# Optimization experiments

Hardware: AMD Instinct MI355X
Metric: run time of the kernel (lower is better)

Reference implementation:

```python
import jax, jax.numpy as jnp
import numpy as np

NEG_SLOPE = 0.2


def _gat_layer(x, edge_index, W, a_src, a_dst, b):
    """PyG GATConv: linear -> per-edge attention logits -> segment softmax over
    destination -> scatter-add weighted messages. Self-loops added (PyG default)."""
    N = x.shape[0]
    heads, out = a_src.shape
    loops = jnp.arange(N, dtype=edge_index.dtype)
    src = jnp.concatenate([edge_index[0], loops])
    dst = jnp.concatenate([edge_index[1], loops])
    xh = (x @ W).reshape(N, heads, out)                      # [N,H,D]
    alpha_s = (xh * a_src).sum(-1)                           # [N,H]
    alpha_d = (xh * a_dst).sum(-1)                           # [N,H]
    e = jax.nn.leaky_relu(alpha_s[src] + alpha_d[dst], NEG_SLOPE)  # [E,H]
    emax = jax.ops.segment_max(e, dst, num_segments=N)       # [N,H]
    ex = jnp.exp(e - emax[dst])
    den = jax.ops.segment_sum(ex, dst, num_segments=N)
    att = ex / (den[dst] + 1e-16)                            # [E,H]
    msg = xh[src] * att[..., None]                           # [E,H,D]
    o = jax.ops.segment_sum(msg, dst, num_segments=N)        # [N,H,D]
    return o.reshape(N, heads * out) + b


def _single_source_gnn(h, edge_index, params):
    n_layers = len(params)
    for i, (W, a_s, a_d, b) in enumerate(params):
        h = _gat_layer(h, edge_index, W, a_s, a_d, b)
        if i < n_layers - 1:
            h = jax.nn.relu(h)
    return h


def setup_inputs() -> dict:
    key = jax.random.key(0)
    B, N, H, heads, deg = 4, 2000, 64, 4, 32
    E = N * deg
    ks = jax.random.split(key, 20)

    def mk_edge_index(k):
        e = jax.random.randint(k, (2, B, E), 0, N)
        off = (jnp.arange(B) * N)[None, :, None]
        return (e + off).reshape(2, B * E).astype(jnp.int32)

    inp = {
        "h0_flat": jax.random.normal(ks[0], (B * N, H), jnp.float32),
        "edge_index_s1": mk_edge_index(ks[1]),
        "edge_index_s2": mk_edge_index(ks[2]),
    }
    dims = [(H, H * heads), (H * heads, H * heads)]
    i = 3
    for s in ("s1", "s2"):
        for l, (din, dout) in enumerate(dims):
            inp[f"W_{s}_{l}"] = jax.random.normal(ks[i], (din, dout), jnp.float32) * 0.1; i += 1
            inp[f"a_src_{s}_{l}"] = jax.random.normal(ks[i], (heads, H), jnp.float32) * 0.1; i += 1
            inp[f"a_dst_{s}_{l}"] = jax.random.normal(ks[i], (heads, H), jnp.float32) * 0.1; i += 1
            inp[f"b_{s}_{l}"] = jnp.zeros((dout,), jnp.float32)
    inp["batch_size"] = B
    inp["num_stocks"] = N
    return inp


def reference(h0_flat, edge_index_s1, edge_index_s2,
              W_s1_0, a_src_s1_0, a_dst_s1_0, b_s1_0,
              W_s1_1, a_src_s1_1, a_dst_s1_1, b_s1_1,
              W_s2_0, a_src_s2_0, a_dst_s2_0, b_s2_0,
              W_s2_1, a_src_s2_1, a_dst_s2_1, b_s2_1,
              batch_size, num_stocks):
    p1 = [(W_s1_0, a_src_s1_0, a_dst_s1_0, b_s1_0),
          (W_s1_1, a_src_s1_1, a_dst_s1_1, b_s1_1)]
    p2 = [(W_s2_0, a_src_s2_0, a_dst_s2_0, b_s2_0),
          (W_s2_1, a_src_s2_1, a_dst_s2_1, b_s2_1)]
    h1 = _single_source_gnn(h0_flat, edge_index_s1, p1)
    h2 = _single_source_gnn(h0_flat, edge_index_s2, p2)
    # dict of per-source outputs in torch -> stacked [n_sources, B*N, H*heads]
    return jnp.stack([h1, h2])
```

## Files before the change

kernel.cpp:

```cpp
#include <hip/hip_runtime.h>
#include <hip/hip_fp16.h>


#define NEG_SLOPE 0.2f
#define ELLW 96

typedef _Float16 half8 __attribute__((ext_vector_type(8)));
typedef float floatx4 __attribute__((ext_vector_type(4)));


__global__ __launch_bounds__(64) void wt_zero_kernel(
        const float* __restrict__ W10, const float* __restrict__ W20,
        const float* __restrict__ W11, const float* __restrict__ W21,
        _Float16* __restrict__ Wt10, _Float16* __restrict__ Wt20,
        _Float16* __restrict__ Wt11, _Float16* __restrict__ Wt21,
        int* __restrict__ cnt, int twoN) {
    int z = blockIdx.z, y = blockIdx.y, c = blockIdx.x;
    int t = threadIdx.x;
    int flat = ((z * gridDim.y + y) * gridDim.x + c) * 64 + t;
    if (flat < twoN) cnt[flat] = 0;
    if (y == 0) {
        const float* W  = z ? W20  : W10;
        _Float16*    Wt = z ? Wt20 : Wt10;
        Wt[(size_t)c * 64 + t] = (_Float16)W[(size_t)t * 256 + c];
    } else {
        int k = (y - 1) * 64 + t;
        const float* W  = z ? W21  : W11;
        _Float16*    Wt = z ? Wt21 : Wt11;
        Wt[(size_t)c * 256 + k] = (_Float16)W[(size_t)k * 256 + c];
    }
}


__global__ __launch_bounds__(256) void scatter_ell_kernel(
        const int* __restrict__ ei1, int E1,
        const int* __restrict__ ei2, int E2, int N,
        int* __restrict__ cnt , int* __restrict__ slots ) {
    int i = blockIdx.x * 256 + threadIdx.x;
    int tot1 = E1 + N;
    int tot2 = E2 + N;
    if (i >= tot1 + tot2) return;
    int s, j; const int* ei; int E;
    if (i < tot1) { s = 0; j = i;        ei = ei1; E = E1; }
    else          { s = 1; j = i - tot1; ei = ei2; E = E2; }
    int src, dst;
    if (j < E) { src = ei[j]; dst = ei[E + j]; }
    else       { src = dst = j - E; }
    int g = s * N + dst;
    int pos = atomicAdd(&cnt[g], 1);
    if (pos < ELLW) slots[(size_t)g * ELLW + pos] = src;
}


#define BK 64
#define HPAD 4

struct GemmArgs {
    const float *h0, *h1;
    const _Float16 *Wt0, *Wt1;
    const float *as0, *as1, *ad0, *ad1;
    __half *xh0, *xh1;
    float *alS0, *alS1, *alD0, *alD1;
    int K;
};

__global__ __launch_bounds__(256) void gemm_mfma_kernel(GemmArgs g) {
    __shared__ _Float16 hT[32][BK + HPAD];
    int s = blockIdx.z;
    const float*    h   = s ? g.h1   : g.h0;
    const _Float16* Wt  = s ? g.Wt1  : g.Wt0;
    const float*    a_s = s ? g.as1  : g.as0;
    const float*    a_d = s ? g.ad1  : g.ad0;
    __half* xh = s ? g.xh1 : g.xh0;
    float* alS = s ? g.alS1 : g.alS0;
    float* alD = s ? g.alD1 : g.alD0;
    const int K = g.K;

    int tid  = threadIdx.x;
    int wave = tid >> 6;
    int lane = tid & 63;
    int lo = lane & 15, hi = lane >> 4;
    int row0 = blockIdx.x * 32;
    int c0 = wave * 64;

    floatx4 acc[2][4] = {};

    int srow = tid >> 3, sseg = tid & 7;
    const float* hrow = h + (size_t)(row0 + srow) * K + sseg * 8;
    const _Float16* wbase = Wt + (size_t)c0 * K;

    for (int k0 = 0; k0 < K; k0 += BK) {
        __syncthreads();
        float4 hv0 = *(const float4*)(hrow + k0);
        float4 hv1 = *(const float4*)(hrow + k0 + 4);
        half8 hh;
        hh[0] = (_Float16)hv0.x; hh[1] = (_Float16)hv0.y;
        hh[2] = (_Float16)hv0.z; hh[3] = (_Float16)hv0.w;
        hh[4] = (_Float16)hv1.x; hh[5] = (_Float16)hv1.y;
        hh[6] = (_Float16)hv1.z; hh[7] = (_Float16)hv1.w;
        *(half8*)&hT[srow][sseg * 8] = hh;
        __syncthreads();

        half8 bf[2][4], af[2][2];
#pragma unroll
        for (int ks = 0; ks < 2; ks++) {
#pragma unroll
            for (int cf = 0; cf < 4; cf++) {
                bf[ks][cf] = *(const half8*)(wbase + (size_t)(cf * 16 + lo) * K
                                             + k0 + ks * 32 + hi * 8);
            }
#pragma unroll
            for (int f = 0; f < 2; f++)
                af[ks][f] = *(const half8*)&hT[f * 16 + lo][ks * 32 + hi * 8];
        }
#pragma unroll
        for (int ks = 0; ks < 2; ks++)
#pragma unroll
            for (int f = 0; f < 2; f++)
#pragma unroll
                for (int cf = 0; cf < 4; cf++)
                    acc[f][cf] = __builtin_amdgcn_mfma_f32_16x16x32_f16(
                        af[ks][f], bf[ks][cf], acc[f][cf], 0, 0, 0);
    }

    float asw[4], adw[4];
#pragma unroll
    for (int cf = 0; cf < 4; cf++) {
        asw[cf] = a_s[c0 + cf * 16 + lo];
        adw[cf] = a_d[c0 + cf * 16 + lo];
    }
#pragma unroll
    for (int f = 0; f < 2; f++) {
#pragma unroll
        for (int r = 0; r < 4; r++) {
            int row = row0 + f * 16 + hi * 4 + r;
            float v0 = acc[f][0][r], v1 = acc[f][1][r];
            float v2 = acc[f][2][r], v3 = acc[f][3][r];
            __half* xrow = &xh[(size_t)row * 256 + c0 + lo];
            xrow[0]  = __float2half(v0);
            xrow[16] = __float2half(v1);
            xrow[32] = __float2half(v2);
            xrow[48] = __float2half(v3);
            float s1 = v0 * asw[0] + v1 * asw[1] + v2 * asw[2] + v3 * asw[3];
            float s2 = v0 * adw[0] + v1 * adw[1] + v2 * adw[2] + v3 * adw[3];
#pragma unroll
            for (int off = 1; off < 16; off <<= 1) {
                s1 += __shfl_xor(s1, off);
                s2 += __shfl_xor(s2, off);
            }
            if (lo == 0) {
                alS[row * 4 + wave] = s1;
                alD[row * 4 + wave] = s2;
            }
        }
    }
}


struct AttnArgs {
    const int *cnt, *slots;
    const __half *xh0, *xh1;
    const float *alS0, *alS1, *alD0, *alD1, *b0, *b1;
    float *out0, *out1;
    int N, do_relu;
};

__global__ __launch_bounds__(256) void attn_kernel(AttnArgs a) {
    __shared__ float2 pairs[4][8][10];
    int tid = threadIdx.x;
    int h  = tid >> 6;
    int L  = tid & 63;
    int st = L >> 3;
    int lc = L & 7;
    int g = blockIdx.x;
    int s = (g >= a.N) ? 1 : 0;
    int dst = g - s * a.N;
    const __half* xh     = s ? a.xh1  : a.xh0;
    const float*  alS    = s ? a.alS1 : a.alS0;
    const float*  alD    = s ? a.alD1 : a.alD0;
    const float*  bias   = s ? a.b1   : a.b0;
    float*        out    = s ? a.out1 : a.out0;

    int nd = a.cnt[g];
    if (nd > ELLW) nd = ELLW;
    const int* slots = a.slots + (size_t)g * ELLW;
    float ad = alD[dst * 4 + h];
    const char* xb = (const char*)xh + h * 128 + lc * 16;

    float acc[8] = {};
    float pden = 0.f;

    for (int c = 0; c < nd; c += 64) {
        int n = nd - c; if (n > 64) n = 64;
        int off = 0; float p = 0.f;
        if (L < n) {
            int src = slots[c + L];
            float t = alS[src * 4 + h] + ad;
            t = (t > 0.f) ? t : NEG_SLOPE * t;
            p = __expf(t);
            off = src * 512;
        }
        pden += p;
        pairs[h][L & 7][L >> 3] = make_float2(__int_as_float(off), p);
        int iters = (n + 7) >> 3;
        for (int ii = 0; ii < iters; ii += 4) {
            float4 twoA = *(const float4*)&pairs[h][st][ii];
            float4 twoB = *(const float4*)&pairs[h][st][ii + 2];
            int   o0 = __float_as_int(twoA.x); float w0 = twoA.y;
            int   o1 = __float_as_int(twoA.z); float w1 = twoA.w;
            int   o2 = __float_as_int(twoB.x); float w2 = twoB.y;
            int   o3 = __float_as_int(twoB.z); float w3 = twoB.w;
            float4 r0 = *(const float4*)(xb + o0);
            float4 r1 = *(const float4*)(xb + o1);
            float4 r2 = *(const float4*)(xb + o2);
            float4 r3 = *(const float4*)(xb + o3);
            const __half2* q0 = (const __half2*)&r0;
            const __half2* q1 = (const __half2*)&r1;
            const __half2* q2 = (const __half2*)&r2;
            const __half2* q3 = (const __half2*)&r3;
#pragma unroll
            for (int k = 0; k < 4; k++) {
                acc[2 * k + 0] += (float)q0[k].x * w0;
                acc[2 * k + 1] += (float)q0[k].y * w0;
            }
#pragma unroll
            for (int k = 0; k < 4; k++) {
                acc[2 * k + 0] += (float)q1[k].x * w1;
                acc[2 * k + 1] += (float)q1[k].y * w1;
            }
#pragma unroll
            for (int k = 0; k < 4; k++) {
                acc[2 * k + 0] += (float)q2[k].x * w2;
                acc[2 * k + 1] += (float)q2[k].y * w2;
            }
#pragma unroll
            for (int k = 0; k < 4; k++) {
                acc[2 * k + 0] += (float)q3[k].x * w3;
                acc[2 * k + 1] += (float)q3[k].y * w3;
            }
        }
    }
#pragma unroll
    for (int k = 0; k < 8; k++) {
        acc[k] += __shfl_xor(acc[k], 8);
        acc[k] += __shfl_xor(acc[k], 16);
        acc[k] += __shfl_xor(acc[k], 32);
    }
#pragma unroll
    for (int o2 = 32; o2 >= 1; o2 >>= 1) pden += __shfl_xor(pden, o2);

    if (st == 0) {
        float d = 1.0f / (pden + 1e-16f);
        int col = h * 64 + lc * 8;
        float4 bA = *(const float4*)&bias[col];
        float4 bB = *(const float4*)&bias[col + 4];
        float4 oA, oB;
        oA.x = acc[0] * d + bA.x; oA.y = acc[1] * d + bA.y;
        oA.z = acc[2] * d + bA.z; oA.w = acc[3] * d + bA.w;
        oB.x = acc[4] * d + bB.x; oB.y = acc[5] * d + bB.y;
        oB.z = acc[6] * d + bB.z; oB.w = acc[7] * d + bB.w;
        if (a.do_relu) {
            oA.x = fmaxf(oA.x, 0.f); oA.y = fmaxf(oA.y, 0.f);
            oA.z = fmaxf(oA.z, 0.f); oA.w = fmaxf(oA.w, 0.f);
            oB.x = fmaxf(oB.x, 0.f); oB.y = fmaxf(oB.y, 0.f);
            oB.z = fmaxf(oB.z, 0.f); oB.w = fmaxf(oB.w, 0.f);
        }
        *(float4*)&out[(size_t)dst * 256 + col] = oA;
        *(float4*)&out[(size_t)dst * 256 + col + 4] = oB;
    }
}


extern "C" void kernel_launch(void* const* d_in, const int* in_sizes, int n_in,
                              void* d_out, int out_size, void* d_ws, size_t ws_size,
                              hipStream_t stream) {
    const float* h0  = (const float*)d_in[0];
    const int*   ei1 = (const int*)d_in[1];
    const int*   ei2 = (const int*)d_in[2];
    const float* W10  = (const float*)d_in[3];
    const float* as10 = (const float*)d_in[4];
    const float* ad10 = (const float*)d_in[5];
    const float* b10  = (const float*)d_in[6];
    const float* W11  = (const float*)d_in[7];
    const float* as11 = (const float*)d_in[8];
    const float* ad11 = (const float*)d_in[9];
    const float* b11  = (const float*)d_in[10];
    const float* W20  = (const float*)d_in[11];
    const float* as20 = (const float*)d_in[12];
    const float* ad20 = (const float*)d_in[13];
    const float* b20  = (const float*)d_in[14];
    const float* W21  = (const float*)d_in[15];
    const float* as21 = (const float*)d_in[16];
    const float* ad21 = (const float*)d_in[17];
    const float* b21  = (const float*)d_in[18];

    const int N  = in_sizes[0] / 64;
    const int E1 = in_sizes[1] / 2;
    const int E2 = in_sizes[2] / 2;

    char* base = (char*)d_ws;
    size_t off = 0;
    auto carve = [&](size_t bytes) -> void* {
        void* p = base + off;
        off += (bytes + 255) & ~(size_t)255;
        return p;
    };
    int* cnt     = (int*)carve((size_t)2 * N * 4);
    int* slots   = (int*)carve((size_t)2 * N * ELLW * 4);
    __half* xh1  = (__half*)carve((size_t)N * 256 * 2);
    __half* xh2  = (__half*)carve((size_t)N * 256 * 2);
    float* hbuf1 = (float*)carve((size_t)N * 256 * 4);
    float* hbuf2 = (float*)carve((size_t)N * 256 * 4);
    float* alS1  = (float*)carve((size_t)N * 4 * 4);
    float* alD1  = (float*)carve((size_t)N * 4 * 4);
    float* alS2  = (float*)carve((size_t)N * 4 * 4);
    float* alD2  = (float*)carve((size_t)N * 4 * 4);
    _Float16* Wt10 = (_Float16*)carve((size_t)256 * 64 * 2);
    _Float16* Wt20 = (_Float16*)carve((size_t)256 * 64 * 2);
    _Float16* Wt11 = (_Float16*)carve((size_t)256 * 256 * 2);
    _Float16* Wt21 = (_Float16*)carve((size_t)256 * 256 * 2);
    (void)ws_size; (void)n_in;

    float* out0 = (float*)d_out;
    float* out1 = (float*)d_out + (size_t)N * 256;

    wt_zero_kernel<<<dim3(256, 5, 2), 64, 0, stream>>>(
        W10, W20, W11, W21, Wt10, Wt20, Wt11, Wt21, cnt, 2 * N);

    int tot = (E1 + N) + (E2 + N);
    scatter_ell_kernel<<<(tot + 255) / 256, 256, 0, stream>>>(
        ei1, E1, ei2, E2, N, cnt, slots);

    const dim3 gemmGrid(N / 32, 1, 2);
    const dim3 attnGrid(2 * N);

    GemmArgs g0 = { h0, h0, Wt10, Wt20, as10, as20, ad10, ad20,
                    xh1, xh2, alS1, alS2, alD1, alD2, 64 };
    AttnArgs a0 = { cnt, slots, xh1, xh2,
                    alS1, alS2, alD1, alD2, b10, b20, hbuf1, hbuf2, N, 1 };
    GemmArgs g1 = { hbuf1, hbuf2, Wt11, Wt21, as11, as21, ad11, ad21,
                    xh1, xh2, alS1, alS2, alD1, alD2, 256 };
    AttnArgs a1 = { cnt, slots, xh1, xh2,
                    alS1, alS2, alD1, alD2, b11, b21, out0, out1, N, 0 };

    gemm_mfma_kernel<<<gemmGrid, 256, 0, stream>>>(g0);
    attn_kernel<<<attnGrid, 256, 0, stream>>>(a0);
    gemm_mfma_kernel<<<gemmGrid, 256, 0, stream>>>(g1);
    attn_kernel<<<attnGrid, 256, 0, stream>>>(a1);
}
```

Measured before the change: 131.4 us.

## Fuse all GAT phases into one cooperative persistent kernel with grid syncs

Merges weight transpose/zeroing, ELL scatter, both GEMMs and both attention passes into a single cooperative kernel separated by grid-wide barriers. Launch overhead and kernel gaps between the six stages are what it targets. The GEMM tile also shrinks from 32 to 16 rows so there are more tiles for the persistent grid to share. It keeps a multi-launch fallback, and the risk is that grid syncs, a grid limited by occupancy, and the persistent loops over 8000 attention nodes may cost more than they save.

```diff
diff --git a/kernel.cpp b/kernel.cpp
--- a/kernel.cpp
+++ b/kernel.cpp
@@ -1,126 +1,112 @@
 #include <hip/hip_runtime.h>
 #include <hip/hip_fp16.h>
+#include <hip/hip_cooperative_groups.h>
+
+namespace cg = cooperative_groups;
 
 
 #define NEG_SLOPE 0.2f
 #define ELLW 96
+#define BK 64
+#define HPAD 8
+#define GROWS 16
 
 typedef _Float16 half8 __attribute__((ext_vector_type(8)));
+typedef _Float16 half4 __attribute__((ext_vector_type(4)));
 typedef float floatx4 __attribute__((ext_vector_type(4)));
 
-
-__global__ __launch_bounds__(64) void wt_zero_kernel(
-        const float* __restrict__ W10, const float* __restrict__ W20,
-        const float* __restrict__ W11, const float* __restrict__ W21,
-        _Float16* __restrict__ Wt10, _Float16* __restrict__ Wt20,
-        _Float16* __restrict__ Wt11, _Float16* __restrict__ Wt21,
-        int* __restrict__ cnt, int twoN) {
-    int z = blockIdx.z, y = blockIdx.y, c = blockIdx.x;
-    int t = threadIdx.x;
-    int flat = ((z * gridDim.y + y) * gridDim.x + c) * 64 + t;
-    if (flat < twoN) cnt[flat] = 0;
-    if (y == 0) {
-        const float* W  = z ? W20  : W10;
-        _Float16*    Wt = z ? Wt20 : Wt10;
-        Wt[(size_t)c * 64 + t] = (_Float16)W[(size_t)t * 256 + c];
-    } else {
-        int k = (y - 1) * 64 + t;
-        const float* W  = z ? W21  : W11;
-        _Float16*    Wt = z ? Wt21 : Wt11;
-        Wt[(size_t)c * 256 + k] = (_Float16)W[(size_t)k * 256 + c];
-    }
-}
-
-
-__global__ __launch_bounds__(256) void scatter_ell_kernel(
-        const int* __restrict__ ei1, int E1,
-        const int* __restrict__ ei2, int E2, int N,
-        int* __restrict__ cnt , int* __restrict__ slots ) {
-    int i = blockIdx.x * 256 + threadIdx.x;
-    int tot1 = E1 + N;
-    int tot2 = E2 + N;
-    if (i >= tot1 + tot2) return;
-    int s, j; const int* ei; int E;
-    if (i < tot1) { s = 0; j = i;        ei = ei1; E = E1; }
-    else          { s = 1; j = i - tot1; ei = ei2; E = E2; }
-    int src, dst;
-    if (j < E) { src = ei[j]; dst = ei[E + j]; }
-    else       { src = dst = j - E; }
-    int g = s * N + dst;
-    int pos = atomicAdd(&cnt[g], 1);
-    if (pos < ELLW) slots[(size_t)g * ELLW + pos] = src;
-}
-
-
-#define BK 64
-#define HPAD 4
-
-struct GemmArgs {
-    const float *h0, *h1;
-    const _Float16 *Wt0, *Wt1;
-    const float *as0, *as1, *ad0, *ad1;
-    __half *xh0, *xh1;
-    float *alS0, *alS1, *alD0, *alD1;
-    int K;
+union SM {
+    _Float16 hT[GROWS][BK + HPAD];
+    float2 pairs[4][8][10];
 };
 
-__global__ __launch_bounds__(256) void gemm_mfma_kernel(GemmArgs g) {
-    __shared__ _Float16 hT[32][BK + HPAD];
-    int s = blockIdx.z;
-    const float*    h   = s ? g.h1   : g.h0;
-    const _Float16* Wt  = s ? g.Wt1  : g.Wt0;
-    const float*    a_s = s ? g.as1  : g.as0;
-    const float*    a_d = s ? g.ad1  : g.ad0;
-    __half* xh = s ? g.xh1 : g.xh0;
-    float* alS = s ? g.alS1 : g.alS0;
-    float* alD = s ? g.alD1 : g.alD0;
-    const int K = g.K;
-
-    int tid  = threadIdx.x;
-    int wave = tid >> 6;
-    int lane = tid & 63;
+struct MegaArgs {
+    const float* h0;
+    const int *ei1, *ei2;
+    const float *W10, *W11, *W20, *W21;
+    const float *as10, *ad10, *b10, *as11, *ad11, *b11;
+    const float *as20, *ad20, *b20, *as21, *ad21, *b21;
+    _Float16 *Wt10, *Wt20, *Wt11, *Wt21;
+    int *cnt, *slots;
+    __half *xh1, *xh2;
+    float *hbuf1, *hbuf2;
+    float *alS1, *alD1, *alS2, *alD2;
+    float *out0, *out1;
+    int N, E1, E2;
+};
+
+
+__device__ __forceinline__ void phase0_body(const MegaArgs& a, int flat, int GT) {
+    for (int i = flat; i < 2 * a.N; i += GT) a.cnt[i] = 0;
+    for (int i = flat; i < 32768; i += GT) {
+        int s = i >> 14, rem = i & 16383;
+        int c = rem >> 6, k = rem & 63;
+        const float* W = s ? a.W20 : a.W10;
+        _Float16* Wt = s ? a.Wt20 : a.Wt10;
+        Wt[c * 64 + k] = (_Float16)W[k * 256 + c];
+    }
+    for (int i = flat; i < 131072; i += GT) {
+        int s = i >> 16, rem = i & 65535;
+        int c = rem >> 8, k = rem & 255;
+        const float* W = s ? a.W21 : a.W11;
+        _Float16* Wt = s ? a.Wt21 : a.Wt11;
+        Wt[c * 256 + k] = (_Float16)W[k * 256 + c];
+    }
+}
+
+
+__device__ __forceinline__ void phase1_body(const MegaArgs& a, int flat, int GT) {
+    int tot1 = a.E1 + a.N, tot2 = a.E2 + a.N;
+    int tot = tot1 + tot2;
+    for (int i = flat; i < tot; i += GT) {
+        int s, j; const int* ei; int E;
+        if (i < tot1) { s = 0; j = i;        ei = a.ei1; E = a.E1; }
+        else          { s = 1; j = i - tot1; ei = a.ei2; E = a.E2; }
+        int src, dst;
+        if (j < E) { src = ei[j]; dst = ei[E + j]; }
+        else       { src = dst = j - E; }
+        int gg = s * a.N + dst;
+        int pos = atomicAdd(&a.cnt[gg], 1);
+        if (pos < ELLW) a.slots[(size_t)gg * ELLW + pos] = src;
+    }
+}
+
+
+__device__ __forceinline__ void gemm_tile(
+        const float* __restrict__ h, const _Float16* __restrict__ Wt,
+        const float* __restrict__ a_s, const float* __restrict__ a_d,
+        __half* __restrict__ xh, float* __restrict__ alS, float* __restrict__ alD,
+        int K, int row0, SM& sm) {
+    int tid = threadIdx.x;
+    int wave = tid >> 6, lane = tid & 63;
     int lo = lane & 15, hi = lane >> 4;
-    int row0 = blockIdx.x * 32;
     int c0 = wave * 64;
-
-    floatx4 acc[2][4] = {};
-
-    int srow = tid >> 3, sseg = tid & 7;
-    const float* hrow = h + (size_t)(row0 + srow) * K + sseg * 8;
+    floatx4 acc[4] = {};
+    int srow = tid >> 4, sseg = tid & 15;
+    const float* hrow = h + (size_t)(row0 + srow) * K + sseg * 4;
     const _Float16* wbase = Wt + (size_t)c0 * K;
 
     for (int k0 = 0; k0 < K; k0 += BK) {
         __syncthreads();
-        float4 hv0 = *(const float4*)(hrow + k0);
-        float4 hv1 = *(const float4*)(hrow + k0 + 4);
-        half8 hh;
-        hh[0] = (_Float16)hv0.x; hh[1] = (_Float16)hv0.y;
-        hh[2] = (_Float16)hv0.z; hh[3] = (_Float16)hv0.w;
-        hh[4] = (_Float16)hv1.x; hh[5] = (_Float16)hv1.y;
-        hh[6] = (_Float16)hv1.z; hh[7] = (_Float16)hv1.w;
-        *(half8*)&hT[srow][sseg * 8] = hh;
+        float4 hv = *(const float4*)(hrow + k0);
+        half4 hh;
+        hh[0] = (_Float16)hv.x; hh[1] = (_Float16)hv.y;
+        hh[2] = (_Float16)hv.z; hh[3] = (_Float16)hv.w;
+        *(half4*)&sm.hT[srow][sseg * 4] = hh;
         __syncthreads();
-
-        half8 bf[2][4], af[2][2];
+        half8 bf[4], af;
 #pragma unroll
         for (int ks = 0; ks < 2; ks++) {
 #pragma unroll
-            for (int cf = 0; cf < 4; cf++) {
-                bf[ks][cf] = *(const half8*)(wbase + (size_t)(cf * 16 + lo) * K
-                                             + k0 + ks * 32 + hi * 8);
-            }
-#pragma unroll
-            for (int f = 0; f < 2; f++)
-                af[ks][f] = *(const half8*)&hT[f * 16 + lo][ks * 32 + hi * 8];
-        }
-#pragma unroll
-        for (int ks = 0; ks < 2; ks++)
-#pragma unroll
-            for (int f = 0; f < 2; f++)
-#pragma unroll
-                for (int cf = 0; cf < 4; cf++)
-                    acc[f][cf] = __builtin_amdgcn_mfma_f32_16x16x32_f16(
-                        af[ks][f], bf[ks][cf], acc[f][cf], 0, 0, 0);
+            for (int cf = 0; cf < 4; cf++)
+                bf[cf] = *(const half8*)(wbase + (size_t)(cf * 16 + lo) * K
+                                         + k0 + ks * 32 + hi * 8);
+            af = *(const half8*)&sm.hT[lo][ks * 32 + hi * 8];
+#pragma unroll
+            for (int cf = 0; cf < 4; cf++)
+                acc[cf] = __builtin_amdgcn_mfma_f32_16x16x32_f16(
+                    af, bf[cf], acc[cf], 0, 0, 0);
+        }
     }
 
     float asw[4], adw[4];
@@ -130,56 +116,62 @@
         adw[cf] = a_d[c0 + cf * 16 + lo];
     }
 #pragma unroll
-    for (int f = 0; f < 2; f++) {
-#pragma unroll
-        for (int r = 0; r < 4; r++) {
-            int row = row0 + f * 16 + hi * 4 + r;
-            float v0 = acc[f][0][r], v1 = acc[f][1][r];
-            float v2 = acc[f][2][r], v3 = acc[f][3][r];
-            __half* xrow = &xh[(size_t)row * 256 + c0 + lo];
-            xrow[0]  = __float2half(v0);
-            xrow[16] = __float2half(v1);
-            xrow[32] = __float2half(v2);
-            xrow[48] = __float2half(v3);
-            float s1 = v0 * asw[0] + v1 * asw[1] + v2 * asw[2] + v3 * asw[3];
-            float s2 = v0 * adw[0] + v1 * adw[1] + v2 * adw[2] + v3 * adw[3];
-#pragma unroll
-            for (int off = 1; off < 16; off <<= 1) {
-                s1 += __shfl_xor(s1, off);
-                s2 += __shfl_xor(s2, off);
-            }
-            if (lo == 0) {
-                alS[row * 4 + wave] = s1;
-                alD[row * 4 + wave] = s2;
-            }
-        }
-    }
-}
-
-
-struct AttnArgs {
-    const int *cnt, *slots;
-    const __half *xh0, *xh1;
-    const float *alS0, *alS1, *alD0, *alD1, *b0, *b1;
-    float *out0, *out1;
-    int N, do_relu;
-};
-
-__global__ __launch_bounds__(256) void attn_kernel(AttnArgs a) {
-    __shared__ float2 pairs[4][8][10];
+    for (int r = 0; r < 4; r++) {
+        int row = row0 + hi * 4 + r;
+        float v0 = acc[0][r], v1 = acc[1][r], v2 = acc[2][r], v3 = acc[3][r];
+        __half* xrow = &xh[(size_t)row * 256 + c0 + lo];
+        xrow[0]  = __float2half(v0);
+        xrow[16] = __float2half(v1);
+        xrow[32] = __float2half(v2);
+        xrow[48] = __float2half(v3);
+        float s1 = v0 * asw[0] + v1 * asw[1] + v2 * asw[2] + v3 * asw[3];
+        float s2 = v0 * adw[0] + v1 * adw[1] + v2 * adw[2] + v3 * adw[3];
+#pragma unroll
+        for (int off = 1; off < 16; off <<= 1) {
+            s1 += __shfl_xor(s1, off);
+            s2 += __shfl_xor(s2, off);
+        }
+        if (lo == 0) {
+            alS[row * 4 + wave] = s1;
+            alD[row * 4 + wave] = s2;
+        }
+    }
+}
+
+__device__ __forceinline__ void gemm_phase(const MegaArgs& a, int layer,
+                                           SM& sm, int bid, int nb) {
+    int half = a.N / GROWS, nt = half * 2;
+    int K = layer ? 256 : 64;
+    for (int u = bid; u < nt; u += nb) {
+        int s = (u >= half);
+        int bx = u - s * half;
+        const float* h = layer ? (s ? a.hbuf2 : a.hbuf1) : a.h0;
+        const _Float16* Wt = layer ? (s ? a.Wt21 : a.Wt11)
+                                   : (s ? a.Wt20 : a.Wt10);
+        const float* as_ = layer ? (s ? a.as21 : a.as11)
+                                 : (s ? a.as20 : a.as10);
+        const float* ad_ = layer ? (s ? a.ad21 : a.ad11)
+                                 : (s ? a.ad20 : a.ad10);
+        gemm_tile(h, Wt, as_, ad_, s ? a.xh2 : a.xh1,
+                  s ? a.alS2 : a.alS1, s ? a.alD2 : a.alD1,
+                  K, bx * GROWS, sm);
+    }
+}
+
+
+__device__ __forceinline__ void attn_node(
+        int g, const MegaArgs& a, const float* __restrict__ b1,
+        const float* __restrict__ b2, float* __restrict__ o1,
+        float* __restrict__ o2, int do_relu, SM& sm) {
     int tid = threadIdx.x;
-    int h  = tid >> 6;
-    int L  = tid & 63;
-    int st = L >> 3;
-    int lc = L & 7;
-    int g = blockIdx.x;
+    int h = tid >> 6, L = tid & 63, st = L >> 3, lc = L & 7;
     int s = (g >= a.N) ? 1 : 0;
     int dst = g - s * a.N;
-    const __half* xh     = s ? a.xh1  : a.xh0;
-    const float*  alS    = s ? a.alS1 : a.alS0;
-    const float*  alD    = s ? a.alD1 : a.alD0;
-    const float*  bias   = s ? a.b1   : a.b0;
-    float*        out    = s ? a.out1 : a.out0;
+    const __half* xh   = s ? a.xh2  : a.xh1;
+    const float*  alS  = s ? a.alS2 : a.alS1;
+    const float*  alD  = s ? a.alD2 : a.alD1;
+    const float*  bias = s ? b2   : b1;
+    float*        out  = s ? o2 : o1;
 
     int nd = a.cnt[g];
     if (nd > ELLW) nd = ELLW;
@@ -201,19 +193,19 @@
             off = src * 512;
         }
         pden += p;
-        pairs[h][L & 7][L >> 3] = make_float2(__int_as_float(off), p);
+        sm.pairs[h][L & 7][L >> 3] = make_float2(__int_as_float(off), p);
         int iters = (n + 7) >> 3;
         for (int ii = 0; ii < iters; ii += 4) {
-            float4 twoA = *(const float4*)&pairs[h][st][ii];
-            float4 twoB = *(const float4*)&pairs[h][st][ii + 2];
-            int   o0 = __float_as_int(twoA.x); float w0 = twoA.y;
-            int   o1 = __float_as_int(twoA.z); float w1 = twoA.w;
-            int   o2 = __float_as_int(twoB.x); float w2 = twoB.y;
-            int   o3 = __float_as_int(twoB.z); float w3 = twoB.w;
-            float4 r0 = *(const float4*)(xb + o0);
-            float4 r1 = *(const float4*)(xb + o1);
-            float4 r2 = *(const float4*)(xb + o2);
-            float4 r3 = *(const float4*)(xb + o3);
+            float4 twoA = *(const float4*)&sm.pairs[h][st][ii];
+            float4 twoB = *(const float4*)&sm.pairs[h][st][ii + 2];
+            int   o0i = __float_as_int(twoA.x); float w0 = twoA.y;
+            int   o1i = __float_as_int(twoA.z); float w1 = twoA.w;
+            int   o2i = __float_as_int(twoB.x); float w2 = twoB.y;
+            int   o3i = __float_as_int(twoB.z); float w3 = twoB.w;
+            float4 r0 = *(const float4*)(xb + o0i);
+            float4 r1 = *(const float4*)(xb + o1i);
+            float4 r2 = *(const float4*)(xb + o2i);
+            float4 r3 = *(const float4*)(xb + o3i);
             const __half2* q0 = (const __half2*)&r0;
             const __half2* q1 = (const __half2*)&r1;
             const __half2* q2 = (const __half2*)&r2;
@@ -222,19 +214,10 @@
             for (int k = 0; k < 4; k++) {
                 acc[2 * k + 0] += (float)q0[k].x * w0;
                 acc[2 * k + 1] += (float)q0[k].y * w0;
-            }
-#pragma unroll
-            for (int k = 0; k < 4; k++) {
                 acc[2 * k + 0] += (float)q1[k].x * w1;
                 acc[2 * k + 1] += (float)q1[k].y * w1;
-            }
-#pragma unroll
-            for (int k = 0; k < 4; k++) {
                 acc[2 * k + 0] += (float)q2[k].x * w2;
                 acc[2 * k + 1] += (float)q2[k].y * w2;
-            }
-#pragma unroll
-            for (int k = 0; k < 4; k++) {
                 acc[2 * k + 0] += (float)q3[k].x * w3;
                 acc[2 * k + 1] += (float)q3[k].y * w3;
             }
@@ -247,7 +230,7 @@
         acc[k] += __shfl_xor(acc[k], 32);
     }
 #pragma unroll
-    for (int o2 = 32; o2 >= 1; o2 >>= 1) pden += __shfl_xor(pden, o2);
+    for (int o2_ = 32; o2_ >= 1; o2_ >>= 1) pden += __shfl_xor(pden, o2_);
 
     if (st == 0) {
         float d = 1.0f / (pden + 1e-16f);
@@ -259,7 +242,7 @@
         oA.z = acc[2] * d + bA.z; oA.w = acc[3] * d + bA.w;
         oB.x = acc[4] * d + bB.x; oB.y = acc[5] * d + bB.y;
         oB.z = acc[6] * d + bB.z; oB.w = acc[7] * d + bB.w;
-        if (a.do_relu) {
+        if (do_relu) {
             oA.x = fmaxf(oA.x, 0.f); oA.y = fmaxf(oA.y, 0.f);
             oA.z = fmaxf(oA.z, 0.f); oA.w = fmaxf(oA.w, 0.f);
             oB.x = fmaxf(oB.x, 0.f); oB.y = fmaxf(oB.y, 0.f);
@@ -268,6 +251,52 @@
         *(float4*)&out[(size_t)dst * 256 + col] = oA;
         *(float4*)&out[(size_t)dst * 256 + col + 4] = oB;
     }
+}
+
+__device__ __forceinline__ void attn_phase(const MegaArgs& a, int layer,
+                                           SM& sm, int bid, int nb) {
+    const float* b1 = layer ? a.b11 : a.b10;
+    const float* b2 = layer ? a.b21 : a.b20;
+    float* o1 = layer ? a.out0 : a.hbuf1;
+    float* o2 = layer ? a.out1 : a.hbuf2;
+    int relu = layer ? 0 : 1;
+    for (int g = bid; g < 2 * a.N; g += nb)
+        attn_node(g, a, b1, b2, o1, o2, relu, sm);
+}
+
+
+__global__ __launch_bounds__(256, 4) void mega_kernel(MegaArgs a) {
+    __shared__ SM sm;
+    cg::grid_group grid = cg::this_grid();
+    int flat = blockIdx.x * 256 + threadIdx.x;
+    int GT = gridDim.x * 256;
+    phase0_body(a, flat, GT);
+    grid.sync();
+    phase1_body(a, flat, GT);
+    grid.sync();
+    gemm_phase(a, 0, sm, blockIdx.x, gridDim.x);
+    grid.sync();
+    attn_phase(a, 0, sm, blockIdx.x, gridDim.x);
+    grid.sync();
+    gemm_phase(a, 1, sm, blockIdx.x, gridDim.x);
+    grid.sync();
+    attn_phase(a, 1, sm, blockIdx.x, gridDim.x);
+}
+
+
+__global__ __launch_bounds__(256) void phase0_k(MegaArgs a) {
+    phase0_body(a, blockIdx.x * 256 + threadIdx.x, gridDim.x * 256);
+}
+__global__ __launch_bounds__(256) void phase1_k(MegaArgs a) {
+    phase1_body(a, blockIdx.x * 256 + threadIdx.x, gridDim.x * 256);
+}
+__global__ __launch_bounds__(256, 4) void gemm_k(MegaArgs a, int layer) {
+    __shared__ SM sm;
+    gemm_phase(a, layer, sm, blockIdx.x, gridDim.x);
+}
+__global__ __launch_bounds__(256, 4) void attn_k(MegaArgs a, int layer) {
+    __shared__ SM sm;
+    attn_phase(a, layer, sm, blockIdx.x, gridDim.x);
 }
 
 
@@ -277,22 +306,6 @@
     const float* h0  = (const float*)d_in[0];
     const int*   ei1 = (const int*)d_in[1];
     const int*   ei2 = (const int*)d_in[2];
-    const float* W10  = (const float*)d_in[3];
-    const float* as10 = (const float*)d_in[4];
-    const float* ad10 = (const float*)d_in[5];
-    const float* b10  = (const float*)d_in[6];
-    const float* W11  = (const float*)d_in[7];
-    const float* as11 = (const float*)d_in[8];
-    const float* ad11 = (const float*)d_in[9];
-    const float* b11  = (const float*)d_in[10];
-    const float* W20  = (const float*)d_in[11];
-    const float* as20 = (const float*)d_in[12];
-    const float* ad20 = (const float*)d_in[13];
-    const float* b20  = (const float*)d_in[14];
-    const float* W21  = (const float*)d_in[15];
-    const float* as21 = (const float*)d_in[16];
-    const float* ad21 = (const float*)d_in[17];
-    const float* b21  = (const float*)d_in[18];
 
     const int N  = in_sizes[0] / 64;
     const int E1 = in_sizes[1] / 2;
@@ -321,30 +334,49 @@
     _Float16* Wt21 = (_Float16*)carve((size_t)256 * 256 * 2);
     (void)ws_size; (void)n_in;
 
-    float* out0 = (float*)d_out;
-    float* out1 = (float*)d_out + (size_t)N * 256;
-
-    wt_zero_kernel<<<dim3(256, 5, 2), 64, 0, stream>>>(
-        W10, W20, W11, W21, Wt10, Wt20, Wt11, Wt21, cnt, 2 * N);
-
-    int tot = (E1 + N) + (E2 + N);
-    scatter_ell_kernel<<<(tot + 255) / 256, 256, 0, stream>>>(
-        ei1, E1, ei2, E2, N, cnt, slots);
-
-    const dim3 gemmGrid(N / 32, 1, 2);
-    const dim3 attnGrid(2 * N);
-
-    GemmArgs g0 = { h0, h0, Wt10, Wt20, as10, as20, ad10, ad20,
-                    xh1, xh2, alS1, alS2, alD1, alD2, 64 };
-    AttnArgs a0 = { cnt, slots, xh1, xh2,
-                    alS1, alS2, alD1, alD2, b10, b20, hbuf1, hbuf2, N, 1 };
-    GemmArgs g1 = { hbuf1, hbuf2, Wt11, Wt21, as11, as21, ad11, ad21,
-                    xh1, xh2, alS1, alS2, alD1, alD2, 256 };
-    AttnArgs a1 = { cnt, slots, xh1, xh2,
-                    alS1, alS2, alD1, alD2, b11, b21, out0, out1, N, 0 };
-
-    gemm_mfma_kernel<<<gemmGrid, 256, 0, stream>>>(g0);
-    attn_kernel<<<attnGrid, 256, 0, stream>>>(a0);
-    gemm_mfma_kernel<<<gemmGrid, 256, 0, stream>>>(g1);
-    attn_kernel<<<attnGrid, 256, 0, stream>>>(a1);
-}
+    MegaArgs a;
+    a.h0 = h0; a.ei1 = ei1; a.ei2 = ei2;
+    a.W10 = (const float*)d_in[3];  a.as10 = (const float*)d_in[4];
+    a.ad10 = (const float*)d_in[5]; a.b10 = (const float*)d_in[6];
+    a.W11 = (const float*)d_in[7];  a.as11 = (const float*)d_in[8];
+    a.ad11 = (const float*)d_in[9]; a.b11 = (const float*)d_in[10];
+    a.W20 = (const float*)d_in[11]; a.as20 = (const float*)d_in[12];
+    a.ad20 = (const float*)d_in[13]; a.b20 = (const float*)d_in[14];
+    a.W21 = (const float*)d_in[15]; a.as21 = (const float*)d_in[16];
+    a.ad21 = (const float*)d_in[17]; a.b21 = (const float*)d_in[18];
+    a.Wt10 = Wt10; a.Wt20 = Wt20; a.Wt11 = Wt11; a.Wt21 = Wt21;
+    a.cnt = cnt; a.slots = slots;
+    a.xh1 = xh1; a.xh2 = xh2;
+    a.hbuf1 = hbuf1; a.hbuf2 = hbuf2;
+    a.alS1 = alS1; a.alD1 = alD1; a.alS2 = alS2; a.alD2 = alD2;
+    a.out0 = (float*)d_out; a.out1 = (float*)d_out + (size_t)N * 256;
+    a.N = N; a.E1 = E1; a.E2 = E2;
+
+    int dev = 0;
+    hipGetDevice(&dev);
+    int coopOK = 0;
+    hipDeviceGetAttribute(&coopOK, hipDeviceAttributeCooperativeLaunch, dev);
+    int cus = 0;
+    hipDeviceGetAttribute(&cus, hipDeviceAttributeMultiprocessorCount, dev);
+    int bpc = 0;
+    hipOccupancyMaxActiveBlocksPerMultiprocessor(&bpc, mega_kernel, 256, 0);
+
+    bool done = false;
+    if (coopOK && bpc > 0 && cus > 0) {
+        int grid = bpc * cus;
+        if (grid > 1024) grid = 1024;
+        void* kargs[] = { (void*)&a };
+        if (hipLaunchCooperativeKernel((const void*)mega_kernel, dim3(grid),
+                                       dim3(256), kargs, 0, stream) == hipSuccess)
+            done = true;
+    }
+    if (!done) {
+        int tot = (E1 + N) + (E2 + N);
+        phase0_k<<<768, 256, 0, stream>>>(a);
+        phase1_k<<<(tot + 255) / 256, 256, 0, stream>>>(a);
+        gemm_k<<<(N / GROWS) * 2, 256, 0, stream>>>(a, 0);
+        attn_k<<<2 * N, 256, 0, stream>>>(a, 0);
+        gemm_k<<<(N / GROWS) * 2, 256, 0, stream>>>(a, 1);
+        attn_k<<<2 * N, 256, 0, stream>>>(a, 1);
+    }
+}
```

After: 522.2 us. +297.4%, slower.

## Fuse layer-0 GEMM with ELL scatter and store hidden activations in fp16

Applied to the files above, without the earlier changes.

Merges the first-layer GEMM and the edge-scatter kernel into one launch, with block ranges split between the two jobs, which removes one kernel launch and lets the two run concurrently. The layer-0 attention output is now written as fp16, so the second GEMM loads half-precision rows directly and skips the fp32-to-fp16 conversion. This halves that intermediate traffic. The LDS padding is also changed and the attention inner loop is merged. The fp16 intermediate adds a rounding step, but the fp32 path already converted to fp16 before the MMA.

```diff
diff --git a/kernel.cpp b/kernel.cpp
--- a/kernel.cpp
+++ b/kernel.cpp
@@ -4,111 +4,91 @@
 
 #define NEG_SLOPE 0.2f
 #define ELLW 96
+#define BK 64
+#define HPAD 8
 
 typedef _Float16 half8 __attribute__((ext_vector_type(8)));
 typedef float floatx4 __attribute__((ext_vector_type(4)));
 
-
-__global__ __launch_bounds__(64) void wt_zero_kernel(
-        const float* __restrict__ W10, const float* __restrict__ W20,
-        const float* __restrict__ W11, const float* __restrict__ W21,
-        _Float16* __restrict__ Wt10, _Float16* __restrict__ Wt20,
-        _Float16* __restrict__ Wt11, _Float16* __restrict__ Wt21,
-        int* __restrict__ cnt, int twoN) {
+struct Args {
+    const float* h0;
+    const int *ei1, *ei2;
+    const float *W10, *W11, *W20, *W21;
+    const float *as10, *ad10, *b10, *as11, *ad11, *b11;
+    const float *as20, *ad20, *b20, *as21, *ad21, *b21;
+    _Float16 *Wt10, *Wt20, *Wt11, *Wt21;
+    int *cnt, *slots;
+    _Float16 *xh1, *xh2;
+    _Float16 *hb1, *hb2;
+    float *alS1, *alD1, *alS2, *alD2;
+    float *out0, *out1;
+    int N, E1, E2, GB0;
+};
+
+
+__global__ __launch_bounds__(64) void wt_zero_kernel(Args a) {
     int z = blockIdx.z, y = blockIdx.y, c = blockIdx.x;
     int t = threadIdx.x;
     int flat = ((z * gridDim.y + y) * gridDim.x + c) * 64 + t;
-    if (flat < twoN) cnt[flat] = 0;
+    if (flat < 2 * a.N) a.cnt[flat] = 0;
     if (y == 0) {
-        const float* W  = z ? W20  : W10;
-        _Float16*    Wt = z ? Wt20 : Wt10;
+        const float* W  = z ? a.W20  : a.W10;
+        _Float16*    Wt = z ? a.Wt20 : a.Wt10;
         Wt[(size_t)c * 64 + t] = (_Float16)W[(size_t)t * 256 + c];
     } else {
         int k = (y - 1) * 64 + t;
-        const float* W  = z ? W21  : W11;
-        _Float16*    Wt = z ? Wt21 : Wt11;
+        const float* W  = z ? a.W21  : a.W11;
+        _Float16*    Wt = z ? a.Wt21 : a.Wt11;
         Wt[(size_t)c * 256 + k] = (_Float16)W[(size_t)k * 256 + c];
     }
 }
 
 
-__global__ __launch_bounds__(256) void scatter_ell_kernel(
-        const int* __restrict__ ei1, int E1,
-        const int* __restrict__ ei2, int E2, int N,
-        int* __restrict__ cnt , int* __restrict__ slots ) {
-    int i = blockIdx.x * 256 + threadIdx.x;
-    int tot1 = E1 + N;
-    int tot2 = E2 + N;
-    if (i >= tot1 + tot2) return;
-    int s, j; const int* ei; int E;
-    if (i < tot1) { s = 0; j = i;        ei = ei1; E = E1; }
-    else          { s = 1; j = i - tot1; ei = ei2; E = E2; }
-    int src, dst;
-    if (j < E) { src = ei[j]; dst = ei[E + j]; }
-    else       { src = dst = j - E; }
-    int g = s * N + dst;
-    int pos = atomicAdd(&cnt[g], 1);
-    if (pos < ELLW) slots[(size_t)g * ELLW + pos] = src;
-}
-
-
-#define BK 64
-#define HPAD 4
-
-struct GemmArgs {
-    const float *h0, *h1;
-    const _Float16 *Wt0, *Wt1;
-    const float *as0, *as1, *ad0, *ad1;
-    __half *xh0, *xh1;
-    float *alS0, *alS1, *alD0, *alD1;
-    int K;
-};
-
-__global__ __launch_bounds__(256) void gemm_mfma_kernel(GemmArgs g) {
-    __shared__ _Float16 hT[32][BK + HPAD];
-    int s = blockIdx.z;
-    const float*    h   = s ? g.h1   : g.h0;
-    const _Float16* Wt  = s ? g.Wt1  : g.Wt0;
-    const float*    a_s = s ? g.as1  : g.as0;
-    const float*    a_d = s ? g.ad1  : g.ad0;
-    __half* xh = s ? g.xh1 : g.xh0;
-    float* alS = s ? g.alS1 : g.alS0;
-    float* alD = s ? g.alD1 : g.alD0;
-    const int K = g.K;
-
+template<bool AHALF>
+__device__ __forceinline__ void gemm_tile(
+        const void* hv, const _Float16* __restrict__ Wt,
+        const float* __restrict__ a_s, const float* __restrict__ a_d,
+        _Float16* __restrict__ xh, float* __restrict__ alS,
+        float* __restrict__ alD, int K, int row0,
+        _Float16 (&hT)[32][BK + HPAD]) {
     int tid  = threadIdx.x;
     int wave = tid >> 6;
     int lane = tid & 63;
     int lo = lane & 15, hi = lane >> 4;
-    int row0 = blockIdx.x * 32;
     int c0 = wave * 64;
 
     floatx4 acc[2][4] = {};
 
     int srow = tid >> 3, sseg = tid & 7;
-    const float* hrow = h + (size_t)(row0 + srow) * K + sseg * 8;
     const _Float16* wbase = Wt + (size_t)c0 * K;
 
     for (int k0 = 0; k0 < K; k0 += BK) {
         __syncthreads();
-        float4 hv0 = *(const float4*)(hrow + k0);
-        float4 hv1 = *(const float4*)(hrow + k0 + 4);
-        half8 hh;
-        hh[0] = (_Float16)hv0.x; hh[1] = (_Float16)hv0.y;
-        hh[2] = (_Float16)hv0.z; hh[3] = (_Float16)hv0.w;
-        hh[4] = (_Float16)hv1.x; hh[5] = (_Float16)hv1.y;
-        hh[6] = (_Float16)hv1.z; hh[7] = (_Float16)hv1.w;
-        *(half8*)&hT[srow][sseg * 8] = hh;
+        if (AHALF) {
+            const _Float16* hrow = (const _Float16*)hv
+                                 + (size_t)(row0 + srow) * K + sseg * 8;
+            *(half8*)&hT[srow][sseg * 8] = *(const half8*)(hrow + k0);
+        } else {
+            const float* hrow = (const float*)hv
+                              + (size_t)(row0 + srow) * K + sseg * 8;
+            float4 hv0 = *(const float4*)(hrow + k0);
+            float4 hv1 = *(const float4*)(hrow + k0 + 4);
+            half8 hh;
+            hh[0] = (_Float16)hv0.x; hh[1] = (_Float16)hv0.y;
+            hh[2] = (_Float16)hv0.z; hh[3] = (_Float16)hv0.w;
+            hh[4] = (_Float16)hv1.x; hh[5] = (_Float16)hv1.y;
+            hh[6] = (_Float16)hv1.z; hh[7] = (_Float16)hv1.w;
+            *(half8*)&hT[srow][sseg * 8] = hh;
+        }
         __syncthreads();
 
         half8 bf[2][4], af[2][2];
 #pragma unroll
         for (int ks = 0; ks < 2; ks++) {
 #pragma unroll
-            for (int cf = 0; cf < 4; cf++) {
+            for (int cf = 0; cf < 4; cf++)
                 bf[ks][cf] = *(const half8*)(wbase + (size_t)(cf * 16 + lo) * K
                                              + k0 + ks * 32 + hi * 8);
-            }
 #pragma unroll
             for (int f = 0; f < 2; f++)
                 af[ks][f] = *(const half8*)&hT[f * 16 + lo][ks * 32 + hi * 8];
@@ -136,11 +116,11 @@
             int row = row0 + f * 16 + hi * 4 + r;
             float v0 = acc[f][0][r], v1 = acc[f][1][r];
             float v2 = acc[f][2][r], v3 = acc[f][3][r];
-            __half* xrow = &xh[(size_t)row * 256 + c0 + lo];
-            xrow[0]  = __float2half(v0);
-            xrow[16] = __float2half(v1);
-            xrow[32] = __float2half(v2);
-            xrow[48] = __float2half(v3);
+            _Float16* xrow = &xh[(size_t)row * 256 + c0 + lo];
+            xrow[0]  = (_Float16)v0;
+            xrow[16] = (_Float16)v1;
+            xrow[32] = (_Float16)v2;
+            xrow[48] = (_Float16)v3;
             float s1 = v0 * asw[0] + v1 * asw[1] + v2 * asw[2] + v3 * asw[3];
             float s2 = v0 * adw[0] + v1 * adw[1] + v2 * adw[2] + v3 * adw[3];
 #pragma unroll
@@ -157,29 +137,61 @@
 }
 
 
-struct AttnArgs {
-    const int *cnt, *slots;
-    const __half *xh0, *xh1;
-    const float *alS0, *alS1, *alD0, *alD1, *b0, *b1;
-    float *out0, *out1;
-    int N, do_relu;
-};
-
-__global__ __launch_bounds__(256) void attn_kernel(AttnArgs a) {
+__global__ __launch_bounds__(256) void g0scat_kernel(Args a) {
+    __shared__ _Float16 hT[32][BK + HPAD];
+    int b = blockIdx.x;
+    if (b < a.GB0) {
+        int half_ = a.GB0 >> 1;
+        int s = (b >= half_);
+        int bx = b - s * half_;
+        gemm_tile<false>(a.h0, s ? a.Wt20 : a.Wt10,
+                         s ? a.as20 : a.as10, s ? a.ad20 : a.ad10,
+                         s ? a.xh2 : a.xh1, s ? a.alS2 : a.alS1,
+                         s ? a.alD2 : a.alD1, 64, bx * 32, hT);
+    } else {
+        int i = (b - a.GB0) * 256 + threadIdx.x;
+        int tot1 = a.E1 + a.N, tot2 = a.E2 + a.N;
+        if (i >= tot1 + tot2) return;
+        int s, j; const int* ei; int E;
+        if (i < tot1) { s = 0; j = i;        ei = a.ei1; E = a.E1; }
+        else          { s = 1; j = i - tot1; ei = a.ei2; E = a.E2; }
+        int src, dst;
+        if (j < E) { src = ei[j]; dst = ei[E + j]; }
+        else       { src = dst = j - E; }
+        int gg = s * a.N + dst;
+        int pos = atomicAdd(&a.cnt[gg], 1);
+        if (pos < ELLW) a.slots[(size_t)gg * ELLW + pos] = src;
+    }
+}
+
+__global__ __launch_bounds__(256) void gemm1_kernel(Args a) {
+    __shared__ _Float16 hT[32][BK + HPAD];
+    int half_ = a.GB0 >> 1;
+    int b = blockIdx.x;
+    int s = (b >= half_);
+    int bx = b - s * half_;
+    gemm_tile<true>(s ? a.hb2 : a.hb1, s ? a.Wt21 : a.Wt11,
+                    s ? a.as21 : a.as11, s ? a.ad21 : a.ad11,
+                    s ? a.xh2 : a.xh1, s ? a.alS2 : a.alS1,
+                    s ? a.alD2 : a.alD1, 256, bx * 32, hT);
+}
+
+
+template<bool OUTHALF>
+__device__ __forceinline__ void attn_impl(
+        const Args& a, const float* __restrict__ b1, const float* __restrict__ b2,
+        void* o1, void* o2, int do_relu) {
     __shared__ float2 pairs[4][8][10];
     int tid = threadIdx.x;
-    int h  = tid >> 6;
-    int L  = tid & 63;
-    int st = L >> 3;
-    int lc = L & 7;
+    int h = tid >> 6, L = tid & 63, st = L >> 3, lc = L & 7;
     int g = blockIdx.x;
     int s = (g >= a.N) ? 1 : 0;
     int dst = g - s * a.N;
-    const __half* xh     = s ? a.xh1  : a.xh0;
-    const float*  alS    = s ? a.alS1 : a.alS0;
-    const float*  alD    = s ? a.alD1 : a.alD0;
-    const float*  bias   = s ? a.b1   : a.b0;
-    float*        out    = s ? a.out1 : a.out0;
+    const _Float16* xh  = s ? a.xh2  : a.xh1;
+    const float*  alS   = s ? a.alS2 : a.alS1;
+    const float*  alD   = s ? a.alD2 : a.alD1;
+    const float*  bias  = s ? b2 : b1;
+    void*         out   = s ? o2 : o1;
 
     int nd = a.cnt[g];
     if (nd > ELLW) nd = ELLW;
@@ -207,13 +219,13 @@
             float4 twoA = *(const float4*)&pairs[h][st][ii];
             float4 twoB = *(const float4*)&pairs[h][st][ii + 2];
             int   o0 = __float_as_int(twoA.x); float w0 = twoA.y;
-            int   o1 = __float_as_int(twoA.z); float w1 = twoA.w;
-            int   o2 = __float_as_int(twoB.x); float w2 = twoB.y;
-            int   o3 = __float_as_int(twoB.z); float w3 = twoB.w;
+            int   o1i = __float_as_int(twoA.z); float w1 = twoA.w;
+            int   o2i = __float_as_int(twoB.x); float w2 = twoB.y;
+            int   o3i = __float_as_int(twoB.z); float w3 = twoB.w;
             float4 r0 = *(const float4*)(xb + o0);
-            float4 r1 = *(const float4*)(xb + o1);
-            float4 r2 = *(const float4*)(xb + o2);
-            float4 r3 = *(const float4*)(xb + o3);
+            float4 r1 = *(const float4*)(xb + o1i);
+            float4 r2 = *(const float4*)(xb + o2i);
+            float4 r3 = *(const float4*)(xb + o3i);
             const __half2* q0 = (const __half2*)&r0;
             const __half2* q1 = (const __half2*)&r1;
             const __half2* q2 = (const __half2*)&r2;
@@ -222,19 +234,10 @@
             for (int k = 0; k < 4; k++) {
                 acc[2 * k + 0] += (float)q0[k].x * w0;
                 acc[2 * k + 1] += (float)q0[k].y * w0;
-            }
-#pragma unroll
-            for (int k = 0; k < 4; k++) {
                 acc[2 * k + 0] += (float)q1[k].x * w1;
                 acc[2 * k + 1] += (float)q1[k].y * w1;
-            }
-#pragma unroll
-            for (int k = 0; k < 4; k++) {
                 acc[2 * k + 0] += (float)q2[k].x * w2;
                 acc[2 * k + 1] += (float)q2[k].y * w2;
-            }
-#pragma unroll
-            for (int k = 0; k < 4; k++) {
                 acc[2 * k + 0] += (float)q3[k].x * w3;
                 acc[2 * k + 1] += (float)q3[k].y * w3;
             }
@@ -247,53 +250,48 @@
         acc[k] += __shfl_xor(acc[k], 32);
     }
 #pragma unroll
-    for (int o2 = 32; o2 >= 1; o2 >>= 1) pden += __shfl_xor(pden, o2);
+    for (int o2_ = 32; o2_ >= 1; o2_ >>= 1) pden += __shfl_xor(pden, o2_);
 
     if (st == 0) {
         float d = 1.0f / (pden + 1e-16f);
         int col = h * 64 + lc * 8;
         float4 bA = *(const float4*)&bias[col];
         float4 bB = *(const float4*)&bias[col + 4];
-        float4 oA, oB;
-        oA.x = acc[0] * d + bA.x; oA.y = acc[1] * d + bA.y;
-        oA.z = acc[2] * d + bA.z; oA.w = acc[3] * d + bA.w;
-        oB.x = acc[4] * d + bB.x; oB.y = acc[5] * d + bB.y;
-        oB.z = acc[6] * d + bB.z; oB.w = acc[7] * d + bB.w;
-        if (a.do_relu) {
-            oA.x = fmaxf(oA.x, 0.f); oA.y = fmaxf(oA.y, 0.f);
-            oA.z = fmaxf(oA.z, 0.f); oA.w = fmaxf(oA.w, 0.f);
-            oB.x = fmaxf(oB.x, 0.f); oB.y = fmaxf(oB.y, 0.f);
-            oB.z = fmaxf(oB.z, 0.f); oB.w = fmaxf(oB.w, 0.f);
-        }
-        *(float4*)&out[(size_t)dst * 256 + col] = oA;
-        *(float4*)&out[(size_t)dst * 256 + col + 4] = oB;
-    }
+        float o[8];
+        o[0] = acc[0] * d + bA.x; o[1] = acc[1] * d + bA.y;
+        o[2] = acc[2] * d + bA.z; o[3] = acc[3] * d + bA.w;
+        o[4] = acc[4] * d + bB.x; o[5] = acc[5] * d + bB.y;
+        o[6] = acc[6] * d + bB.z; o[7] = acc[7] * d + bB.w;
+        if (do_relu) {
+#pragma unroll
+            for (int k = 0; k < 8; k++) o[k] = fmaxf(o[k], 0.f);
+        }
+        if (OUTHALF) {
+            half8 ov;
+#pragma unroll
+            for (int k = 0; k < 8; k++) ov[k] = (_Float16)o[k];
+            *(half8*)((_Float16*)out + (size_t)dst * 256 + col) = ov;
+        } else {
+            float4 oA, oB;
+            oA.x = o[0]; oA.y = o[1]; oA.z = o[2]; oA.w = o[3];
+            oB.x = o[4]; oB.y = o[5]; oB.z = o[6]; oB.w = o[7];
+            *(float4*)((float*)out + (size_t)dst * 256 + col) = oA;
+            *(float4*)((float*)out + (size_t)dst * 256 + col + 4) = oB;
+        }
+    }
+}
+
+__global__ __launch_bounds__(256) void attn0_kernel(Args a) {
+    attn_impl<true>(a, a.b10, a.b20, a.hb1, a.hb2, 1);
+}
+__global__ __launch_bounds__(256) void attn1_kernel(Args a) {
+    attn_impl<false>(a, a.b11, a.b21, a.out0, a.out1, 0);
 }
 
 
 extern "C" void kernel_launch(void* const* d_in, const int* in_sizes, int n_in,
                               void* d_out, int out_size, void* d_ws, size_t ws_size,
                               hipStream_t stream) {
-    const float* h0  = (const float*)d_in[0];
-    const int*   ei1 = (const int*)d_in[1];
-    const int*   ei2 = (const int*)d_in[2];
-    const float* W10  = (const float*)d_in[3];
-    const float* as10 = (const float*)d_in[4];
-    const float* ad10 = (const float*)d_in[5];
-    const float* b10  = (const float*)d_in[6];
-    const float* W11  = (const float*)d_in[7];
-    const float* as11 = (const float*)d_in[8];
-    const float* ad11 = (const float*)d_in[9];
-    const float* b11  = (const float*)d_in[10];
-    const float* W20  = (const float*)d_in[11];
-    const float* as20 = (const float*)d_in[12];
-    const float* ad20 = (const float*)d_in[13];
-    const float* b20  = (const float*)d_in[14];
-    const float* W21  = (const float*)d_in[15];
-    const float* as21 = (const float*)d_in[16];
-    const float* ad21 = (const float*)d_in[17];
-    const float* b21  = (const float*)d_in[18];
-
     const int N  = in_sizes[0] / 64;
     const int E1 = in_sizes[1] / 2;
     const int E2 = in_sizes[2] / 2;
@@ -305,46 +303,48 @@
         off += (bytes + 255) & ~(size_t)255;
         return p;
     };
-    int* cnt     = (int*)carve((size_t)2 * N * 4);
-    int* slots   = (int*)carve((size_t)2 * N * ELLW * 4);
-    __half* xh1  = (__half*)carve((size_t)N * 256 * 2);
-    __half* xh2  = (__half*)carve((size_t)N * 256 * 2);
-    float* hbuf1 = (float*)carve((size_t)N * 256 * 4);
-    float* hbuf2 = (float*)carve((size_t)N * 256 * 4);
-    float* alS1  = (float*)carve((size_t)N * 4 * 4);
-    float* alD1  = (float*)carve((size_t)N * 4 * 4);
-    float* alS2  = (float*)carve((size_t)N * 4 * 4);
-    float* alD2  = (float*)carve((size_t)N * 4 * 4);
-    _Float16* Wt10 = (_Float16*)carve((size_t)256 * 64 * 2);
-    _Float16* Wt20 = (_Float16*)carve((size_t)256 * 64 * 2);
-    _Float16* Wt11 = (_Float16*)carve((size_t)256 * 256 * 2);
-    _Float16* Wt21 = (_Float16*)carve((size_t)256 * 256 * 2);
+    int* cnt        = (int*)carve((size_t)2 * N * 4);
+    int* slots      = (int*)carve((size_t)2 * N * ELLW * 4);
+    _Float16* xh1   = (_Float16*)carve((size_t)N * 256 * 2);
+    _Float16* xh2   = (_Float16*)carve((size_t)N * 256 * 2);
+    _Float16* hb1   = (_Float16*)carve((size_t)N * 256 * 2);
+    _Float16* hb2   = (_Float16*)carve((size_t)N * 256 * 2);
+    float* alS1     = (float*)carve((size_t)N * 4 * 4);
+    float* alD1     = (float*)carve((size_t)N * 4 * 4);
+    float* alS2     = (float*)carve((size_t)N * 4 * 4);
+    float* alD2     = (float*)carve((size_t)N * 4 * 4);
+    _Float16* Wt10  = (_Float16*)carve((size_t)256 * 64 * 2);
+    _Float16* Wt20  = (_Float16*)carve((size_t)256 * 64 * 2);
+    _Float16* Wt11  = (_Float16*)carve((size_t)256 * 256 * 2);
+    _Float16* Wt21  = (_Float16*)carve((size_t)256 * 256 * 2);
     (void)ws_size; (void)n_in;
 
-    float* out0 = (float*)d_out;
-    float* out1 = (float*)d_out + (size_t)N * 256;
-
-    wt_zero_kernel<<<dim3(256, 5, 2), 64, 0, stream>>>(
-        W10, W20, W11, W21, Wt10, Wt20, Wt11, Wt21, cnt, 2 * N);
+    Args a;
+    a.h0 = (const float*)d_in[0];
+    a.ei1 = (const int*)d_in[1];
+    a.ei2 = (const int*)d_in[2];
+    a.W10 = (const float*)d_in[3];  a.as10 = (const float*)d_in[4];
+    a.ad10 = (const float*)d_in[5]; a.b10 = (const float*)d_in[6];
+    a.W11 = (const float*)d_in[7];  a.as11 = (const float*)d_in[8];
+    a.ad11 = (const float*)d_in[9]; a.b11 = (const float*)d_in[10];
+    a.W20 = (const float*)d_in[11]; a.as20 = (const float*)d_in[12];
+    a.ad20 = (const float*)d_in[13]; a.b20 = (const float*)d_in[14];
+    a.W21 = (const float*)d_in[15]; a.as21 = (const float*)d_in[16];
+    a.ad21 = (const float*)d_in[17]; a.b21 = (const float*)d_in[18];
+    a.Wt10 = Wt10; a.Wt20 = Wt20; a.Wt11 = Wt11; a.Wt21 = Wt21;
+    a.cnt = cnt; a.slots = slots;
+    a.xh1 = xh1; a.xh2 = xh2; a.hb1 = hb1; a.hb2 = hb2;
+    a.alS1 = alS1; a.alD1 = alD1; a.alS2 = alS2; a.alD2 = alD2;
+    a.out0 = (float*)d_out; a.out1 = (float*)d_out + (size_t)N * 256;
+    a.N = N; a.E1 = E1; a.E2 = E2;
+    a.GB0 = (N / 32) * 2;
 
     int tot = (E1 + N) + (E2 + N);
-    scatter_ell_kernel<<<(tot + 255) / 256, 256, 0, stream>>>(
-        ei1, E1, ei2, E2, N, cnt, slots);
-
-    const dim3 gemmGrid(N / 32, 1, 2);
-    const dim3 attnGrid(2 * N);
-
-    GemmArgs g0 = { h0, h0, Wt10, Wt20, as10, as20, ad10, ad20,
-                    xh1, xh2, alS1, alS2, alD1, alD2, 64 };
-    AttnArgs a0 = { cnt, slots, xh1, xh2,
-                    alS1, alS2, alD1, alD2, b10, b20, hbuf1, hbuf2, N, 1 };
-    GemmArgs g1 = { hbuf1, hbuf2, Wt11, Wt21, as11, as21, ad11, ad21,
-                    xh1, xh2, alS1, alS2, alD1, alD2, 256 };
-    AttnArgs a1 = { cnt, slots, xh1, xh2,
-                    alS1, alS2, alD1, alD2, b11, b21, out0, out1, N, 0 };
-
-    gemm_mfma_kernel<<<gemmGrid, 256, 0, stream>>>(g0);
-    attn_kernel<<<attnGrid, 256, 0, stream>>>(a0);
-    gemm_mfma_kernel<<<gemmGrid, 256, 0, stream>>>(g1);
-    attn_kernel<<<attnGrid, 256, 0, stream>>>(a1);
-}
+    int scatterBlocks = (tot + 255) / 256;
+
+    wt_zero_kernel<<<dim3(256, 5, 2), 64, 0, stream>>>(a);
+    g0scat_kernel<<<a.GB0 + scatterBlocks, 256, 0, stream>>>(a);
+    attn0_kernel<<<2 * N, 256, 0, stream>>>(a);
+    gemm1_kernel<<<a.GB0, 256, 0, stream>>>(a);
+    attn1_kernel<<<2 * N, 256, 0, stream>>>(a);
+}
```

Result: faster. 121.6 us (-7.5%).
